# Optimization experiments

Measured on AMD Instinct MI355X. Metric: run time of the kernel, lower is better.

The kernel has to match this reference:

```python
import jax, jax.numpy as jnp
import numpy as np

B, S, D, H = 2, 2048, 2048, 16
HD = D // H                     # head_dim = 128
ROTARY_BASE = 10000.0
CAP = 50.0                      # self.cap = FloatTensor([50.0])
FMIN = float(np.finfo(np.float32).min)
SCALE = 1.0 / np.sqrt(HD).astype(np.float32)


def _rope_sincos(seq_len, dim):
    # fixed_pos_embedding_factory with scaling_factor=1, no expand
    inv_freq = 1.0 / ROTARY_BASE ** (2.0 * jnp.arange(dim // 2, dtype=jnp.float32) / dim)
    pos = jnp.arange(seq_len, dtype=jnp.float32)
    ang = pos[:, None] * inv_freq[None, :]          # [S, dim/2]
    return jnp.sin(ang), jnp.cos(ang)


def _apply_rotary(x, sin, cos):
    # x: [B,S,H,hd]; sin/cos: [S,hd/2]. duplicate_interleave is a no-op
    # (view(-1,1).repeat(1,1).view(dim0,-1) returns m unchanged), so this is
    # NeoX-style (split-half) rotary.
    sin = sin[None, :, None, :]
    cos = cos[None, :, None, :]
    x1, x2 = jnp.split(x, 2, axis=-1)
    return jnp.concatenate([x1 * cos - x2 * sin, x2 * cos + x1 * sin], axis=-1)


def setup_inputs() -> dict:
    key = jax.random.key(0)
    kx, kq, kk, kv, ko = jax.random.split(key, 5)
    w = 0.02
    return {
        "x":  jax.random.normal(kx, (B, S, D), jnp.float32),
        "Wq": jax.random.normal(kq, (D, D), jnp.float32) * w,
        "Wk": jax.random.normal(kk, (D, D), jnp.float32) * w,
        "Wv": jax.random.normal(kv, (D, D), jnp.float32) * w,
        "Wo": jax.random.normal(ko, (D, D), jnp.float32) * w,
    }


def reference(x, Wq, Wk, Wv, Wo):
    # projections (bias=False)
    q = (x @ Wq).reshape(B, S, H, HD)
    k = (x @ Wk).reshape(B, S, H, HD)
    v = (x @ Wv).reshape(B, S, H, HD)

    # rotary over the full head dim (rotary_pct = 1.0)
    sin, cos = _rope_sincos(S, HD)
    q = _apply_rotary(q, sin, cos)
    k = _apply_rotary(k, sin, cos)

    # [B,H,S,hd]
    q = q.transpose(0, 2, 1, 3)
    k = k.transpose(0, 2, 1, 3)
    v = v.transpose(0, 2, 1, 3)

    # scores [B,H,S,S]
    scores = jnp.einsum("bhqd,bhkd->bhqk", q, k) * SCALE

    # logit cap: cap * tanh(x / cap)
    scores = CAP * jnp.tanh(scores / CAP)

    # causal mask (tril bias buffer), masked to finfo.min
    causal = jnp.tril(jnp.ones((S, S), dtype=bool))
    scores = jnp.where(causal[None, None], scores, FMIN)

    # LingvoSoftmax: softmax with an extra zero logit appended per row
    m = jnp.maximum(jnp.max(scores, axis=-1, keepdims=True), 0.0)
    e = jnp.exp(scores - m)
    denom = jnp.sum(e, axis=-1, keepdims=True) + jnp.exp(-m)
    probs = e / denom

    out = jnp.einsum("bhqk,bhkd->bhqd", probs, v)      # [B,H,S,hd]
    out = out.transpose(0, 2, 1, 3).reshape(B, S, D)
    return out @ Wo
```

## Files before the change

kernel.cpp:

```cpp
#include <hip/hip_runtime.h>
#include <hip/hip_bf16.h>

#define B_  2
#define S_  2048
#define D_  2048
#define H_  16
#define HD_ 128

typedef unsigned short u16;
typedef __attribute__((ext_vector_type(8))) short bf16x8;
typedef __attribute__((ext_vector_type(4))) float f32x4;
typedef __attribute__((ext_vector_type(16))) float f32x16;

#define GLOAD_LDS16(g, l)                                                     \
  __builtin_amdgcn_global_load_lds(                                           \
      (const __attribute__((address_space(1))) void*)(g),                     \
      (__attribute__((address_space(3))) void*)(l), 16, 0, 0)

__device__ __forceinline__ u16 f2bf(float f){
  unsigned u; __builtin_memcpy(&u, &f, 4);
  u += 0x7fffu + ((u >> 16) & 1u);
  return (u16)(u >> 16);
}
__device__ __forceinline__ float bf2f(u16 h){
  unsigned u = ((unsigned)h) << 16; float f; __builtin_memcpy(&f, &u, 4); return f;
}
__device__ __forceinline__ unsigned pack_bf16x2(float lo, float hi){
  __hip_bfloat162 h2 = __float22bfloat162_rn(float2{lo, hi});
  unsigned u; __builtin_memcpy(&u, &h2, 4); return u;
}

__global__ void cast_x_kernel(const float* __restrict__ x, u16* __restrict__ xb){
  int i = blockIdx.x * 256 + threadIdx.x;
  float4 v = reinterpret_cast<const float4*>(x)[i];
  ushort4 o; o.x = f2bf(v.x); o.y = f2bf(v.y); o.z = f2bf(v.z); o.w = f2bf(v.w);
  reinterpret_cast<ushort4*>(xb)[i] = o;
}

__global__ void wtrans_kernel(const float* __restrict__ w0, const float* __restrict__ w1,
                              const float* __restrict__ w2, const float* __restrict__ w3,
                              u16* __restrict__ o0, u16* __restrict__ o1,
                              u16* __restrict__ o2, u16* __restrict__ o3){
  __shared__ float t[32][33];
  const float* src; u16* dst;
  switch (blockIdx.z){
    case 0:  src = w0; dst = o0; break;
    case 1:  src = w1; dst = o1; break;
    case 2:  src = w2; dst = o2; break;
    default: src = w3; dst = o3; break;
  }
  int j0 = blockIdx.x * 32, i0 = blockIdx.y * 32;
  int tx = threadIdx.x & 31, ty = threadIdx.x >> 5;
  #pragma unroll
  for (int rr = 0; rr < 4; ++rr)
    t[ty + rr*8][tx] = src[(size_t)(i0 + ty + rr*8) * D_ + j0 + tx];
  __syncthreads();
  #pragma unroll
  for (int rr = 0; rr < 4; ++rr)
    dst[(size_t)(j0 + ty + rr*8) * D_ + i0 + tx] = f2bf(t[tx][ty + rr*8]);
}

template<int MODE>
__global__ __launch_bounds__(256) void gemm128_kernel(
    const u16* __restrict__ A,
    const u16* __restrict__ B0, const u16* __restrict__ B1, const u16* __restrict__ B2,
    u16* __restrict__ qb, u16* __restrict__ kb, u16* __restrict__ vtb,
    float* __restrict__ outp)
{
  constexpr int K = 2048;
  __shared__ u16 As[128 * 32];
  __shared__ u16 Bs[128 * 32];
  int m0 = blockIdx.x * 128;
  int by = blockIdx.y;
  int which, n0;
  const u16* Bmat;
  if (MODE == 0){ which = by >> 4; n0 = (by & 15) * 128;
                  Bmat = (which == 0) ? B0 : ((which == 1) ? B1 : B2); }
  else          { which = 0; n0 = by * 128; Bmat = B0; }

  int tid  = threadIdx.x;
  int lane = tid & 63;
  int wid  = tid >> 6;
  int wr = wid >> 1, wc = wid & 1;
  int g = lane >> 4, r = lane & 15;

  f32x4 zero = {0.f, 0.f, 0.f, 0.f};
  f32x4 acc[4][4];
  #pragma unroll
  for (int i = 0; i < 4; ++i)
    #pragma unroll
    for (int j = 0; j < 4; ++j) acc[i][j] = zero;

  for (int kt = 0; kt < K; kt += 32){
    #pragma unroll
    for (int jj = 0; jj < 2; ++jj){
      int cbase = wid * 64 + jj * 256;
      int c  = cbase + lane;
      int rr = c >> 2, c8 = c & 3;
      GLOAD_LDS16(&A[(size_t)(m0 + rr) * K + kt + c8 * 8],    &As[cbase * 8]);
      GLOAD_LDS16(&Bmat[(size_t)(n0 + rr) * K + kt + c8 * 8], &Bs[cbase * 8]);
    }
    asm volatile("s_waitcnt vmcnt(0)" ::: "memory");
    __syncthreads();
    bf16x8 af[4], bfr[4];
    #pragma unroll
    for (int i = 0; i < 4; ++i)
      af[i]  = *reinterpret_cast<bf16x8*>(&As[(wr*64 + i*16 + r) * 32 + g * 8]);
    #pragma unroll
    for (int i = 0; i < 4; ++i)
      bfr[i] = *reinterpret_cast<bf16x8*>(&Bs[(wc*64 + i*16 + r) * 32 + g * 8]);
    #pragma unroll
    for (int i = 0; i < 4; ++i)
      #pragma unroll
      for (int j = 0; j < 4; ++j)
        acc[i][j] = __builtin_amdgcn_mfma_f32_16x16x32_bf16(af[i], bfr[j], acc[i][j], 0, 0, 0);
    __syncthreads();
  }

  #pragma unroll
  for (int i = 0; i < 4; ++i){
    int row0 = m0 + wr*64 + i*16 + g*4;
    int b  = row0 >> 11, s0 = row0 & (S_ - 1);
    #pragma unroll
    for (int j = 0; j < 4; ++j){
      int col = n0 + wc*64 + j*16 + r;
      if (MODE == 1){
        #pragma unroll
        for (int e = 0; e < 4; ++e)
          outp[(size_t)(row0 + e) * D_ + col] = acc[i][j][e];
      } else {
        int h = col >> 7, d = col & 127;
        int bh = b * H_ + h;
        if (which == 2){
          ushort4 pk;
          pk.x = f2bf(acc[i][j][0]); pk.y = f2bf(acc[i][j][1]);
          pk.z = f2bf(acc[i][j][2]); pk.w = f2bf(acc[i][j][3]);
          *reinterpret_cast<ushort4*>(&vtb[((size_t)bh * HD_ + d) * S_ + s0]) = pk;
        } else {
          u16* dstb = (which == 0) ? qb : kb;
          #pragma unroll
          for (int e = 0; e < 4; ++e)
            dstb[((size_t)bh * S_ + s0 + e) * HD_ + d] = f2bf(acc[i][j][e]);
        }
      }
    }
  }
}

__global__ void rope_kernel(u16* __restrict__ qbuf, u16* __restrict__ kbuf){
  int idx = blockIdx.x * 256 + threadIdx.x;
  int j  = idx & 63;
  int s  = (idx >> 6) & (S_ - 1);
  int bh = idx >> 17;
  const float LOG2_1E4 = 13.287712379549449f;
  float inv = exp2f(-(float)(2 * j) * (LOG2_1E4 / 128.f));
  float ang = (float)s * inv;
  float sn = __sinf(ang), cs = __cosf(ang);
  size_t base = ((size_t)bh * S_ + s) * HD_;
  float x1 = bf2f(qbuf[base + j]), x2 = bf2f(qbuf[base + 64 + j]);
  qbuf[base + j]      = f2bf(x1 * cs - x2 * sn);
  qbuf[base + 64 + j] = f2bf(x2 * cs + x1 * sn);
  float y1 = bf2f(kbuf[base + j]), y2 = bf2f(kbuf[base + 64 + j]);
  kbuf[base + j]      = f2bf(y1 * cs - y2 * sn);
  kbuf[base + 64 + j] = f2bf(y2 * cs + y1 * sn);
}

__global__ __launch_bounds__(256) void attn5_kernel(
  const u16* __restrict__ qbuf, const u16* __restrict__ kbuf,
  const u16* __restrict__ vtb,  u16* __restrict__ ob)
{
  __shared__ u16 Klds[2][32 * 128];
  __shared__ u16 Vlds[2][128 * 32];

  const int lane = threadIdx.x & 63;
  const int wid  = threadIdx.x >> 6;
  const int r    = lane & 31;
  const int hi   = lane >> 5;
  const int bh   = blockIdx.x;
  const int qblk = 15 - blockIdx.y;
  const int qc   = qblk * 128 + wid * 32;
  const int cend = 4 * qblk + wid;
  const int tmax = 4 * qblk + 3;

  const float SCALE = 0.08838834764831845f;

  const size_t sbase = (size_t)bh * S_ * HD_;
  const size_t vbase = (size_t)bh * HD_ * S_;

  bf16x8 qf[8];
  {
    const u16* qrow = qbuf + sbase + (size_t)(qc + r) * HD_ + hi * 8;
    #pragma unroll
    for (int cc = 0; cc < 8; ++cc)
      qf[cc] = *reinterpret_cast<const bf16x8*>(qrow + cc * 16);
  }

  f32x16 oacc[4];
  #pragma unroll
  for (int i = 0; i < 4; ++i)
    #pragma unroll
    for (int j = 0; j < 16; ++j) oacc[i][j] = 0.f;
  float lsum = 0.f;

  auto stage = [&](int buf, int t){
    const int kv0 = t * 32;
    u16* Kt = &Klds[buf][0];
    u16* Vt = &Vlds[buf][0];
    #pragma unroll
    for (int j = 0; j < 2; ++j){
      const int cbase = wid * 64 + j * 256;
      const int ck = cbase + lane;
      const int krow = ck >> 4, kslot = ck & 15;
      GLOAD_LDS16(kbuf + sbase + (size_t)(kv0 + krow) * HD_ + ((kslot ^ (krow & 15)) * 8),
                  Kt + cbase * 8);
      const int vd = ck >> 2, vslot = ck & 3;
      GLOAD_LDS16(vtb + vbase + (size_t)vd * S_ + kv0 + ((vslot ^ ((vd >> 1) & 3)) * 8),
                  Vt + cbase * 8);
    }
  };

  stage(0, 0);
  asm volatile("s_waitcnt vmcnt(0)" ::: "memory");
  __syncthreads();

  for (int t = 0; t <= tmax; ++t){
    const int cur = t & 1;
    if (t < tmax) stage(cur ^ 1, t + 1);

    if (t <= cend){
      const bool diag = (t == cend);
      f32x16 sc;
      #pragma unroll
      for (int j = 0; j < 16; ++j) sc[j] = 0.f;
      const u16* Kt = &Klds[cur][0];
      #pragma unroll
      for (int cc = 0; cc < 8; ++cc){
        const int slot = (cc * 2 + hi) ^ (r & 15);
        bf16x8 kf = *reinterpret_cast<const bf16x8*>(&Kt[r * 128 + slot * 8]);
        sc = __builtin_amdgcn_mfma_f32_32x32x16_bf16(kf, qf[cc], sc, 0, 0, 0);
      }
      float p[16];
      #pragma unroll
      for (int reg = 0; reg < 16; ++reg){
        float tt = sc[reg] * SCALE;
        float u  = tt * tt * 4.0e-4f;
        float capped = tt * (1.f - u * 0.33333333f + u * u * 0.13333333f);
        float pv = __expf(capped);
        if (diag){
          int kl = (reg & 3) + 8 * (reg >> 2) + 4 * hi;
          if (kl > r) pv = 0.f;
        }
        p[reg] = pv;
        lsum += pv;
      }
      unsigned a[4], b[4];
      #pragma unroll
      for (int r4 = 0; r4 < 4; ++r4){
        a[r4] = pack_bf16x2(p[r4*4+0], p[r4*4+1]);
        b[r4] = pack_bf16x2(p[r4*4+2], p[r4*4+3]);
      }
      unsigned ra0 = __shfl_xor(hi ? a[0] : a[1], 32);
      unsigned rb0 = __shfl_xor(hi ? b[0] : b[1], 32);
      unsigned ra1 = __shfl_xor(hi ? a[2] : a[3], 32);
      unsigned rb1 = __shfl_xor(hi ? b[2] : b[3], 32);
      unsigned pw[8];
      pw[0] = hi ? ra0 : a[0];  pw[1] = hi ? rb0 : b[0];
      pw[2] = hi ? a[1] : ra0;  pw[3] = hi ? b[1] : rb0;
      pw[4] = hi ? ra1 : a[2];  pw[5] = hi ? rb1 : b[2];
      pw[6] = hi ? a[3] : ra1;  pw[7] = hi ? b[3] : rb1;
      bf16x8 pb0, pb1;
      __builtin_memcpy(&pb0, &pw[0], 16);
      __builtin_memcpy(&pb1, &pw[4], 16);
      const u16* Vt = &Vlds[cur][0];
      #pragma unroll
      for (int i = 0; i < 4; ++i){
        const int d  = i * 32 + r;
        const int sw = (d >> 1) & 3;
        bf16x8 vf0 = *reinterpret_cast<const bf16x8*>(&Vt[d * 32 + (hi ^ sw) * 8]);
        oacc[i] = __builtin_amdgcn_mfma_f32_32x32x16_bf16(vf0, pb0, oacc[i], 0, 0, 0);
        bf16x8 vf1 = *reinterpret_cast<const bf16x8*>(&Vt[d * 32 + ((2 + hi) ^ sw) * 8]);
        oacc[i] = __builtin_amdgcn_mfma_f32_32x32x16_bf16(vf1, pb1, oacc[i], 0, 0, 0);
      }
    }
    asm volatile("s_waitcnt vmcnt(0)" ::: "memory");
    __syncthreads();
  }

  float lt = lsum + __shfl_xor(lsum, 32);
  float linv = 1.0f / (1.0f + lt);

  const int b = bh >> 4, h = bh & 15;
  u16* orow = ob + ((size_t)(b * S_ + qc + r)) * D_ + h * HD_;
  #pragma unroll
  for (int i = 0; i < 4; ++i){
    #pragma unroll
    for (int r4 = 0; r4 < 4; ++r4){
      ushort4 st;
      st.x = f2bf(oacc[i][r4*4+0] * linv);
      st.y = f2bf(oacc[i][r4*4+1] * linv);
      st.z = f2bf(oacc[i][r4*4+2] * linv);
      st.w = f2bf(oacc[i][r4*4+3] * linv);
      *reinterpret_cast<ushort4*>(orow + i*32 + r4*8 + hi*4) = st;
    }
  }
}

extern "C" void kernel_launch(void* const* d_in, const int* in_sizes, int n_in,
                              void* d_out, int out_size, void* d_ws, size_t ws_size,
                              hipStream_t stream){
  const float* x  = (const float*)d_in[0];
  const float* Wq = (const float*)d_in[1];
  const float* Wk = (const float*)d_in[2];
  const float* Wv = (const float*)d_in[3];
  const float* Wo = (const float*)d_in[4];
  float* out = (float*)d_out;
  char* ws = (char*)d_ws;

  u16* xb   = (u16*)(ws);
  u16* wtq  = (u16*)(ws + (size_t)(16u << 20));
  u16* wtk  = (u16*)(ws + (size_t)(24u << 20));
  u16* wtv  = (u16*)(ws + (size_t)(32u << 20));
  u16* wto  = (u16*)(ws + (size_t)(40u << 20));
  u16* qbuf = (u16*)(ws + (size_t)(48u << 20));
  u16* kbuf = (u16*)(ws + (size_t)(64u << 20));
  u16* vtb  = (u16*)(ws + (size_t)(80u << 20));
  u16* atb  = (u16*)(ws + (size_t)(96u << 20));

  cast_x_kernel<<<8192, 256, 0, stream>>>(x, xb);
  wtrans_kernel<<<dim3(64, 64, 4), 256, 0, stream>>>(Wq, Wk, Wv, Wo, wtq, wtk, wtv, wto);
  gemm128_kernel<0><<<dim3(32, 48), 256, 0, stream>>>(xb, wtq, wtk, wtv,
                                                      qbuf, kbuf, vtb, nullptr);
  rope_kernel<<<16384, 256, 0, stream>>>(qbuf, kbuf);
  attn5_kernel<<<dim3(32, 16), 256, 0, stream>>>(qbuf, kbuf, vtb, atb);
  gemm128_kernel<1><<<dim3(32, 16), 256, 0, stream>>>(atb, wto, nullptr, nullptr,
                                                      nullptr, nullptr, nullptr, out);
}
```

Measured before the change: 308.9 us.

## Use 64-key KV tiles in attention and XCD-aware block mapping in GEMMs

The attention kernel now stages 64 keys per pipeline step instead of 32 and processes two 32-key subtiles per stage. This halves the number of barrier and wait cycles per query block, with the V LDS swizzle reworked for the wider tile. The GEMMs switch to a 1D grid whose block index is remapped so blocks on the same XCD share weight N-columns, aiming for better L2 reuse. The cost is double the LDS for attention (64KB), which may lower occupancy, plus extra wasted work on partially masked tiles.

```diff
diff --git a/kernel.cpp b/kernel.cpp
--- a/kernel.cpp
+++ b/kernel.cpp
@@ -70,8 +70,12 @@
   constexpr int K = 2048;
   __shared__ u16 As[128 * 32];
   __shared__ u16 Bs[128 * 32];
-  int m0 = blockIdx.x * 128;
-  int by = blockIdx.y;
+  const int bid = blockIdx.x;
+  const int xcd = bid & 7, loc = bid >> 3;
+  const int mq  = loc & 31;
+  const int nl  = loc >> 5;
+  const int by  = (MODE == 0) ? (xcd * 6 + nl) : (xcd * 2 + nl);
+  const int m0  = mq * 128;
   int which, n0;
   const u16* Bmat;
   if (MODE == 0){ which = by >> 4; n0 = (by & 15) * 128;
@@ -165,12 +169,12 @@
   kbuf[base + 64 + j] = f2bf(y2 * cs + y1 * sn);
 }
 
-__global__ __launch_bounds__(256) void attn5_kernel(
+__global__ __launch_bounds__(256) void attn6_kernel(
   const u16* __restrict__ qbuf, const u16* __restrict__ kbuf,
   const u16* __restrict__ vtb,  u16* __restrict__ ob)
 {
-  __shared__ u16 Klds[2][32 * 128];
-  __shared__ u16 Vlds[2][128 * 32];
+  __shared__ u16 Klds[2][64 * 128];
+  __shared__ u16 Vlds[2][128 * 64];
 
   const int lane = threadIdx.x & 63;
   const int wid  = threadIdx.x >> 6;
@@ -179,8 +183,8 @@
   const int bh   = blockIdx.x;
   const int qblk = 15 - blockIdx.y;
   const int qc   = qblk * 128 + wid * 32;
-  const int cend = 4 * qblk + wid;
-  const int tmax = 4 * qblk + 3;
+  const int qc32 = qc >> 5;
+  const int T    = 2 * qblk + 2;
 
   const float SCALE = 0.08838834764831845f;
 
@@ -203,18 +207,18 @@
   float lsum = 0.f;
 
   auto stage = [&](int buf, int t){
-    const int kv0 = t * 32;
+    const int kv0 = t * 64;
     u16* Kt = &Klds[buf][0];
     u16* Vt = &Vlds[buf][0];
     #pragma unroll
-    for (int j = 0; j < 2; ++j){
-      const int cbase = wid * 64 + j * 256;
+    for (int j = 0; j < 4; ++j){
+      const int cbase = j * 256 + wid * 64;
       const int ck = cbase + lane;
       const int krow = ck >> 4, kslot = ck & 15;
       GLOAD_LDS16(kbuf + sbase + (size_t)(kv0 + krow) * HD_ + ((kslot ^ (krow & 15)) * 8),
                   Kt + cbase * 8);
-      const int vd = ck >> 2, vslot = ck & 3;
-      GLOAD_LDS16(vtb + vbase + (size_t)vd * S_ + kv0 + ((vslot ^ ((vd >> 1) & 3)) * 8),
+      const int vd = ck >> 3, vslot = ck & 7;
+      GLOAD_LDS16(vtb + vbase + (size_t)vd * S_ + kv0 + ((vslot ^ (vd & 7)) * 8),
                   Vt + cbase * 8);
     }
   };
@@ -223,63 +227,70 @@
   asm volatile("s_waitcnt vmcnt(0)" ::: "memory");
   __syncthreads();
 
-  for (int t = 0; t <= tmax; ++t){
+  for (int t = 0; t < T; ++t){
     const int cur = t & 1;
-    if (t < tmax) stage(cur ^ 1, t + 1);
-
-    if (t <= cend){
-      const bool diag = (t == cend);
-      f32x16 sc;
-      #pragma unroll
-      for (int j = 0; j < 16; ++j) sc[j] = 0.f;
-      const u16* Kt = &Klds[cur][0];
-      #pragma unroll
-      for (int cc = 0; cc < 8; ++cc){
-        const int slot = (cc * 2 + hi) ^ (r & 15);
-        bf16x8 kf = *reinterpret_cast<const bf16x8*>(&Kt[r * 128 + slot * 8]);
-        sc = __builtin_amdgcn_mfma_f32_32x32x16_bf16(kf, qf[cc], sc, 0, 0, 0);
-      }
-      float p[16];
-      #pragma unroll
-      for (int reg = 0; reg < 16; ++reg){
-        float tt = sc[reg] * SCALE;
-        float u  = tt * tt * 4.0e-4f;
-        float capped = tt * (1.f - u * 0.33333333f + u * u * 0.13333333f);
-        float pv = __expf(capped);
-        if (diag){
-          int kl = (reg & 3) + 8 * (reg >> 2) + 4 * hi;
-          if (kl > r) pv = 0.f;
-        }
-        p[reg] = pv;
-        lsum += pv;
-      }
-      unsigned a[4], b[4];
-      #pragma unroll
-      for (int r4 = 0; r4 < 4; ++r4){
-        a[r4] = pack_bf16x2(p[r4*4+0], p[r4*4+1]);
-        b[r4] = pack_bf16x2(p[r4*4+2], p[r4*4+3]);
-      }
-      unsigned ra0 = __shfl_xor(hi ? a[0] : a[1], 32);
-      unsigned rb0 = __shfl_xor(hi ? b[0] : b[1], 32);
-      unsigned ra1 = __shfl_xor(hi ? a[2] : a[3], 32);
-      unsigned rb1 = __shfl_xor(hi ? b[2] : b[3], 32);
-      unsigned pw[8];
-      pw[0] = hi ? ra0 : a[0];  pw[1] = hi ? rb0 : b[0];
-      pw[2] = hi ? a[1] : ra0;  pw[3] = hi ? b[1] : rb0;
-      pw[4] = hi ? ra1 : a[2];  pw[5] = hi ? rb1 : b[2];
-      pw[6] = hi ? a[3] : ra1;  pw[7] = hi ? b[3] : rb1;
-      bf16x8 pb0, pb1;
-      __builtin_memcpy(&pb0, &pw[0], 16);
-      __builtin_memcpy(&pb1, &pw[4], 16);
-      const u16* Vt = &Vlds[cur][0];
-      #pragma unroll
-      for (int i = 0; i < 4; ++i){
-        const int d  = i * 32 + r;
-        const int sw = (d >> 1) & 3;
-        bf16x8 vf0 = *reinterpret_cast<const bf16x8*>(&Vt[d * 32 + (hi ^ sw) * 8]);
-        oacc[i] = __builtin_amdgcn_mfma_f32_32x32x16_bf16(vf0, pb0, oacc[i], 0, 0, 0);
-        bf16x8 vf1 = *reinterpret_cast<const bf16x8*>(&Vt[d * 32 + ((2 + hi) ^ sw) * 8]);
-        oacc[i] = __builtin_amdgcn_mfma_f32_32x32x16_bf16(vf1, pb1, oacc[i], 0, 0, 0);
+    if (t + 1 < T) stage(cur ^ 1, t + 1);
+
+    const u16* Kt = &Klds[cur][0];
+    const u16* Vt = &Vlds[cur][0];
+    #pragma unroll
+    for (int sub = 0; sub < 2; ++sub){
+      const int t32 = 2 * t + sub;
+      if (t32 <= qc32){
+        const bool diag = (t32 == qc32);
+        f32x16 sc;
+        #pragma unroll
+        for (int j = 0; j < 16; ++j) sc[j] = 0.f;
+        #pragma unroll
+        for (int cc = 0; cc < 8; ++cc){
+          const int row = sub * 32 + r;
+          const int slot = (cc * 2 + hi) ^ (r & 15);
+          bf16x8 kf = *reinterpret_cast<const bf16x8*>(&Kt[row * 128 + slot * 8]);
+          sc = __builtin_amdgcn_mfma_f32_32x32x16_bf16(kf, qf[cc], sc, 0, 0, 0);
+        }
+        float p[16];
+        #pragma unroll
+        for (int reg = 0; reg < 16; ++reg){
+          float tt = sc[reg] * SCALE;
+          float u  = tt * tt * 4.0e-4f;
+          float capped = tt * (1.f - u * 0.33333333f + u * u * 0.13333333f);
+          float pv = __expf(capped);
+          if (diag){
+            int kl = (reg & 3) + 8 * (reg >> 2) + 4 * hi;
+            if (kl > r) pv = 0.f;
+          }
+          p[reg] = pv;
+          lsum += pv;
+        }
+        unsigned a[4], b[4];
+        #pragma unroll
+        for (int r4 = 0; r4 < 4; ++r4){
+          a[r4] = pack_bf16x2(p[r4*4+0], p[r4*4+1]);
+          b[r4] = pack_bf16x2(p[r4*4+2], p[r4*4+3]);
+        }
+        unsigned ra0 = __shfl_xor(hi ? a[0] : a[1], 32);
+        unsigned rb0 = __shfl_xor(hi ? b[0] : b[1], 32);
+        unsigned ra1 = __shfl_xor(hi ? a[2] : a[3], 32);
+        unsigned rb1 = __shfl_xor(hi ? b[2] : b[3], 32);
+        unsigned pw[8];
+        pw[0] = hi ? ra0 : a[0];  pw[1] = hi ? rb0 : b[0];
+        pw[2] = hi ? a[1] : ra0;  pw[3] = hi ? b[1] : rb0;
+        pw[4] = hi ? ra1 : a[2];  pw[5] = hi ? rb1 : b[2];
+        pw[6] = hi ? a[3] : ra1;  pw[7] = hi ? b[3] : rb1;
+        bf16x8 pb0, pb1;
+        __builtin_memcpy(&pb0, &pw[0], 16);
+        __builtin_memcpy(&pb1, &pw[4], 16);
+        #pragma unroll
+        for (int i = 0; i < 4; ++i){
+          const int d  = i * 32 + r;
+          const int sw = d & 7;
+          bf16x8 vf0 = *reinterpret_cast<const bf16x8*>(
+              &Vt[d * 64 + (((sub * 4 + hi) ^ sw) * 8)]);
+          oacc[i] = __builtin_amdgcn_mfma_f32_32x32x16_bf16(vf0, pb0, oacc[i], 0, 0, 0);
+          bf16x8 vf1 = *reinterpret_cast<const bf16x8*>(
+              &Vt[d * 64 + (((sub * 4 + 2 + hi) ^ sw) * 8)]);
+          oacc[i] = __builtin_amdgcn_mfma_f32_32x32x16_bf16(vf1, pb1, oacc[i], 0, 0, 0);
+        }
       }
     }
     asm volatile("s_waitcnt vmcnt(0)" ::: "memory");
@@ -328,10 +339,10 @@
 
   cast_x_kernel<<<8192, 256, 0, stream>>>(x, xb);
   wtrans_kernel<<<dim3(64, 64, 4), 256, 0, stream>>>(Wq, Wk, Wv, Wo, wtq, wtk, wtv, wto);
-  gemm128_kernel<0><<<dim3(32, 48), 256, 0, stream>>>(xb, wtq, wtk, wtv,
-                                                      qbuf, kbuf, vtb, nullptr);
+  gemm128_kernel<0><<<1536, 256, 0, stream>>>(xb, wtq, wtk, wtv,
+                                              qbuf, kbuf, vtb, nullptr);
   rope_kernel<<<16384, 256, 0, stream>>>(qbuf, kbuf);
-  attn5_kernel<<<dim3(32, 16), 256, 0, stream>>>(qbuf, kbuf, vtb, atb);
-  gemm128_kernel<1><<<dim3(32, 16), 256, 0, stream>>>(atb, wto, nullptr, nullptr,
-                                                      nullptr, nullptr, nullptr, out);
-}
+  attn6_kernel<<<dim3(32, 16), 256, 0, stream>>>(qbuf, kbuf, vtb, atb);
+  gemm128_kernel<1><<<512, 256, 0, stream>>>(atb, wto, nullptr, nullptr,
+                                             nullptr, nullptr, nullptr, out);
+}
```

Result: faster. 292.3 us (-5.4%).
